# Optimization experiments

Hardware: AMD Instinct MI355X
Metric: run time of the kernel (lower is better)

The kernel has to match this reference:

```python
import jax, jax.numpy as jnp
import numpy as np

KS = (16, 16, 16)  # k per layer

def _knn_idx(pts, k):
    # pts: (P, C). Exclude self (knn_graph default loop=False).
    P = pts.shape[0]
    sq = jnp.sum(pts * pts, axis=1)
    d2 = sq[:, None] + sq[None, :] - 2.0 * (pts @ pts.T)  # (P, P)
    d2 = d2.at[jnp.arange(P), jnp.arange(P)].set(jnp.inf)
    _, idx = jax.lax.top_k(-d2, k)  # (P, k) nearest neighbors
    return idx

def _edge_conv(h, idx, W, b):
    # h: (P, C); idx: (P, k); W: (2C, Cout)
    hi = h[:, None, :]                      # (P, 1, C)
    hj = h[idx]                             # (P, k, C) gather
    msg = jnp.concatenate([jnp.broadcast_to(hi, hj.shape), hj - hi], axis=-1)
    m = msg @ W + b                         # (P, k, Cout)
    return jnp.max(m, axis=1)               # max aggregation -> (P, Cout)

def setup_inputs() -> dict:
    key = jax.random.key(0)
    ks = jax.random.split(key, 12)
    B, N, d = 2, 4096, 3
    chans = [d, 64, 128, 256]
    inp = {"x": jax.random.normal(ks[0], (B, N, d), dtype=jnp.float32)}
    for i in range(3):
        cin, cout = chans[i], chans[i + 1]
        s = 1.0 / np.sqrt(2 * cin)
        inp[f"W{i+1}"] = jax.random.uniform(ks[1 + 2 * i], (2 * cin, cout), jnp.float32, -s, s)
        inp[f"b{i+1}"] = jax.random.uniform(ks[2 + 2 * i], (cout,), jnp.float32, -s, s)
    s1 = 1.0 / np.sqrt(256.0)
    inp["fW1"] = jax.random.uniform(ks[7], (256, 128), jnp.float32, -s1, s1)
    inp["fb1"] = jax.random.uniform(ks[8], (128,), jnp.float32, -s1, s1)
    s2 = 1.0 / np.sqrt(128.0)
    inp["fW2"] = jax.random.uniform(ks[9], (128, 1), jnp.float32, -s2, s2)
    inp["fb2"] = jax.random.uniform(ks[10], (1,), jnp.float32, -s2, s2)
    return inp

def reference(x, W1, b1, W2, b2, W3, b3, fW1, fb1, fW2, fb2):
    B, N, _ = x.shape
    h = x.reshape(B * N, -1)  # KNN spans flattened batch (batch=None in source)
    for (W, b, k) in ((W1, b1, KS[0]), (W2, b2, KS[1]), (W3, b3, KS[2])):
        idx = _knn_idx(h, k)
        h = jax.nn.relu(_edge_conv(h, idx, W, b))
    out = jax.nn.relu(h @ fW1 + fb1) @ fW2 + fb2  # (P, 1)
    return out.reshape(B, N, 1)
```

## Files before the change

kernel.cpp:

```cpp
#include <hip/hip_runtime.h>
#include <hip/hip_bf16.h>

#define PTS 8192
#define NSPLIT 8

__device__ __forceinline__ void top_init(float (&bd)[16], int (&bi)[16]) {
#pragma unroll
  for (int t = 0; t < 16; ++t) { bd[t] = 3e38f; bi[t] = 0; }
}

__device__ __forceinline__ void top_insert(float (&bd)[16], int (&bi)[16], float d, int j) {
  if (d < bd[15]) {
#pragma unroll
    for (int t = 15; t >= 0; --t) {
      bool c  = d < bd[t];
      bool cp = (t > 0) ? (d < bd[t - 1]) : false;
      float nd = cp ? bd[t - 1] : d;
      int   ni = cp ? bi[t - 1] : j;
      if (c) { bd[t] = nd; bi[t] = ni; }
    }
  }
}

__global__ void sqnorm_kernel(const float* __restrict__ h, float* __restrict__ sq, int C) {
  int i = blockIdx.x * 256 + threadIdx.x;
  if (i >= PTS) return;
  const float* r = h + (size_t)i * C;
  float s = 0.f;
  if ((C & 3) == 0) {
    for (int k = 0; k < C; k += 4) {
      float4 v = *(const float4*)(r + k);
      s += v.x * v.x + v.y * v.y + v.z * v.z + v.w * v.w;
    }
  } else {
    for (int k = 0; k < C; ++k) s += r[k] * r[k];
  }
  sq[i] = s;
}

template <int C>
__global__ __launch_bounds__(128) void knn_kernel(const float* __restrict__ H,
                                                  const float* __restrict__ sq,
                                                  float* __restrict__ pd,
                                                  int* __restrict__ pi) {
  constexpr int KC = (C < 32) ? C : 32;
  constexpr int NC = C / KC;
  constexpr int TT = (PTS / NSPLIT) / 64;
  constexpr int N  = TT * NC;

  __shared__ __align__(128) float AsF[C * 64];
  __shared__ __align__(128) float S[2 * 32 * 64];

  const int tid  = threadIdx.x;
  const int b    = blockIdx.x;
  const int sy   = b & 7;
  const int sx   = b >> 3;
  const int row0 = sx * 64;
  const int cb   = sy * (PTS / NSPLIT);
  const int tx = tid & 15, ty = tid >> 4;
  const int r_ = tid & 63, g_ = tid >> 6;

  if constexpr (C >= 32) {
    const int r = tid >> 1, h = tid & 1;
#pragma unroll
    for (int j = 0; j < C / 8; ++j) {
      int q = h * (C / 8) + j;
      float4 v = *(const float4*)(H + (size_t)(row0 + r) * C + q * 4);
      float vv[4] = {v.x, v.y, v.z, v.w};
#pragma unroll
      for (int e = 0; e < 4; ++e)
        AsF[(q * 4 + e) * 64 + r] = vv[e];
    }
  } else {
    if (tid < 16 * C) {
      float4 v = *(const float4*)(H + (size_t)row0 * C + tid * 4);
      float vv[4] = {v.x, v.y, v.z, v.w};
#pragma unroll
      for (int e = 0; e < 4; ++e) {
        int gi = tid * 4 + e;
        AsF[(gi % C) * 64 + gi / C] = vv[e];
      }
    }
  }

  float sqr[8];
#pragma unroll
  for (int u = 0; u < 8; ++u) sqr[u] = sq[row0 + ty * 8 + u];

  float bd[16]; int bi[16];
  top_init(bd, bi);

  float4 st[4];
#pragma unroll
  for (int j = 0; j < 4; ++j) st[j] = make_float4(0.f, 0.f, 0.f, 0.f);

  auto stage_load = [&](int n1) {
    if constexpr (C >= 32) {
      const int c = tid & 63, kq = tid >> 6;
      const float* src = H + (size_t)(cb + (n1 / NC) * 64 + c) * C + (n1 % NC) * KC + kq * 16;
#pragma unroll
      for (int j = 0; j < 4; ++j) st[j] = *(const float4*)(src + j * 4);
    } else {
      if (tid < 16 * C) st[0] = *(const float4*)(H + (size_t)(cb + n1 * 64) * C + tid * 4);
    }
  };
  auto stage_write = [&](int n1) {
    float* B = S + (n1 & 1) * 2048;
    if constexpr (C >= 32) {
      const int c = tid & 63, kq = tid >> 6;
#pragma unroll
      for (int j = 0; j < 4; ++j) {
        float vv[4] = {st[j].x, st[j].y, st[j].z, st[j].w};
#pragma unroll
        for (int e = 0; e < 4; ++e)
          B[(kq * 16 + j * 4 + e) * 64 + c] = vv[e];
      }
    } else {
      if (tid < 16 * C) {
        float vv[4] = {st[0].x, st[0].y, st[0].z, st[0].w};
#pragma unroll
        for (int e = 0; e < 4; ++e) {
          int gi = tid * 4 + e;
          B[(gi % C) * 64 + gi / C] = vv[e];
        }
      }
    }
  };

  stage_load(0);
  stage_write(0);
  __syncthreads();

  float acc[8][4] = {};
  for (int n = 0; n < N; ++n) {
    if (n + 1 < N) stage_load(n + 1);
    const float* Bh = S + (n & 1) * 2048;
    const int kc = (n % NC) * KC;
#pragma unroll
    for (int k = 0; k < KC; ++k) {
      float4 a40 = *(const float4*)(AsF + (kc + k) * 64 + ty * 8);
      float4 a41 = *(const float4*)(AsF + (kc + k) * 64 + ty * 8 + 4);
      float4 b4  = *(const float4*)(Bh + k * 64 + tx * 4);
      float a[8]  = {a40.x, a40.y, a40.z, a40.w, a41.x, a41.y, a41.z, a41.w};
      float bb[4] = {b4.x, b4.y, b4.z, b4.w};
#pragma unroll
      for (int u = 0; u < 8; ++u)
#pragma unroll
        for (int v = 0; v < 4; ++v)
          acc[u][v] += a[u] * bb[v];
    }
    if ((n % NC) == NC - 1) {
      const int ct = (n / NC) * 64;
      const int cbase = cb + ct;
      float sqc[4];
#pragma unroll
      for (int v = 0; v < 4; ++v) sqc[v] = sq[cbase + tx * 4 + v];
      __syncthreads();
#pragma unroll
      for (int u = 0; u < 8; ++u) {
        int row = ty * 8 + u;
        int gr  = row0 + row;
        int sw  = (row & 7) << 2;
        float dv[4];
#pragma unroll
        for (int v = 0; v < 4; ++v) {
          float d2 = sqr[u] + sqc[v] - 2.f * acc[u][v];
          if (gr == cbase + tx * 4 + v) d2 = 3e38f;
          dv[v] = d2;
          acc[u][v] = 0.f;
        }
        *(float4*)(S + row * 64 + ((tx * 4) ^ sw)) = make_float4(dv[0], dv[1], dv[2], dv[3]);
      }
      __syncthreads();
      const int swr = (r_ & 7) << 2;
      unsigned mask = 0;
#pragma unroll
      for (int j = 0; j < 8; ++j) {
        float4 f = *(const float4*)(S + r_ * 64 + ((g_ * 32 + j * 4) ^ swr));
        if (f.x < bd[15]) mask |= (1u << (j * 4 + 0));
        if (f.y < bd[15]) mask |= (1u << (j * 4 + 1));
        if (f.z < bd[15]) mask |= (1u << (j * 4 + 2));
        if (f.w < bd[15]) mask |= (1u << (j * 4 + 3));
      }
      while (mask) {
        int q = __ffs(mask) - 1;
        mask &= mask - 1;
        int cc = g_ * 32 + q;
        float d = S[r_ * 64 + (cc ^ swr)];
        top_insert(bd, bi, d, cbase + cc);
      }
      __syncthreads();
    }
    if (n + 1 < N) {
      stage_write(n + 1);
      __syncthreads();
    }
  }

  __syncthreads();
  if (g_ == 1) {
    float* base = S + r_ * 32;
#pragma unroll
    for (int t = 0; t < 16; ++t) {
      int s = (t + r_) & 15;
      base[s] = bd[t];
      ((int*)base)[16 + s] = bi[t];
    }
  }
  __syncthreads();
  if (g_ == 0) {
    const float* base = S + r_ * 32;
    for (int t = 0; t < 16; ++t) {
      int s = (t + r_) & 15;
      float d = base[s];
      if (d >= bd[15]) break;
      top_insert(bd, bi, d, ((const int*)base)[16 + s]);
    }
    size_t basep = ((size_t)(row0 + r_) * NSPLIT + sy) * 16;
#pragma unroll
    for (int t = 0; t < 16; ++t) { pd[basep + t] = bd[t]; pi[basep + t] = bi[t]; }
  }
}

__global__ void knn_merge_kernel(const float* __restrict__ pd, const int* __restrict__ pi,
                                 int* __restrict__ idx) {
  int i = blockIdx.x * 256 + threadIdx.x;
  if (i >= PTS) return;
  float bd[16]; int bi[16];
  top_init(bd, bi);
  const float* d  = pd + (size_t)i * (NSPLIT * 16);
  const int*   ii = pi + (size_t)i * (NSPLIT * 16);
  for (int L = 0; L < NSPLIT; ++L) {
    for (int t = 0; t < 16; ++t) {
      float dv = d[L * 16 + t];
      if (dv >= bd[15]) break;
      top_insert(bd, bi, dv, ii[L * 16 + t]);
    }
  }
#pragma unroll
  for (int t = 0; t < 16; ++t) idx[(size_t)i * 16 + t] = bi[t];
}

__global__ __launch_bounds__(256) void gemm_fg_kernel(const float* __restrict__ A,
                                                      const float* __restrict__ Wt,
                                                      const float* __restrict__ Wb,
                                                      const float* __restrict__ bias,
                                                      float* __restrict__ F, float* __restrict__ G,
                                                      int K, int N) {
  __shared__ float As[16][68];
  __shared__ float Bs[16][68];
  const int tid  = threadIdx.x;
  const int row0 = blockIdx.x * 64, col0 = blockIdx.y * 64;
  const float* B = (blockIdx.z == 0) ? Wt : Wb;
  float* O       = (blockIdx.z == 0) ? F  : G;
  const int tx = tid & 15, ty = tid >> 4;
  float acc[4][4] = {};
  for (int k0 = 0; k0 < K; k0 += 16) {
    __syncthreads();
#pragma unroll
    for (int l = 0; l < 4; ++l) {
      int rr = (tid >> 4) + l * 16, kk = tid & 15;
      As[kk][rr] = (k0 + kk < K) ? A[(size_t)(row0 + rr) * K + k0 + kk] : 0.f;
      int cc = tid & 63, k2 = (tid >> 6) + l * 4;
      Bs[k2][cc] = (k0 + k2 < K) ? B[(size_t)(k0 + k2) * N + col0 + cc] : 0.f;
    }
    __syncthreads();
#pragma unroll
    for (int k = 0; k < 16; ++k) {
      float4 a4 = *(const float4*)&As[k][ty * 4];
      float4 b4 = *(const float4*)&Bs[k][tx * 4];
      float a[4] = {a4.x, a4.y, a4.z, a4.w};
      float b[4] = {b4.x, b4.y, b4.z, b4.w};
#pragma unroll
      for (int u = 0; u < 4; ++u)
#pragma unroll
        for (int v = 0; v < 4; ++v)
          acc[u][v] += a[u] * b[v];
    }
  }
  float bv[4] = {0.f, 0.f, 0.f, 0.f};
  if (blockIdx.z == 0) {
#pragma unroll
    for (int v = 0; v < 4; ++v) bv[v] = bias[col0 + tx * 4 + v];
  }
#pragma unroll
  for (int u = 0; u < 4; ++u)
#pragma unroll
    for (int v = 0; v < 4; ++v)
      O[(size_t)(row0 + ty * 4 + u) * N + col0 + tx * 4 + v] = acc[u][v] + bv[v];
}

__global__ void gather_max_kernel(const float* __restrict__ F, const float* __restrict__ G,
                                  const int* __restrict__ idx, float* __restrict__ Ho, int Cn) {
  int t = blockIdx.x * 256 + threadIdx.x;
  int per = Cn >> 2;
  int i = t / per;
  if (i >= PTS) return;
  int c = (t - i * per) * 4;
  const int* ji = idx + (size_t)i * 16;
  float4 m = make_float4(-3e38f, -3e38f, -3e38f, -3e38f);
#pragma unroll
  for (int s = 0; s < 16; ++s) {
    float4 v = *(const float4*)(G + (size_t)ji[s] * Cn + c);
    m.x = fmaxf(m.x, v.x); m.y = fmaxf(m.y, v.y);
    m.z = fmaxf(m.z, v.z); m.w = fmaxf(m.w, v.w);
  }
  float4 gi = *(const float4*)(G + (size_t)i * Cn + c);
  float4 f  = *(const float4*)(F + (size_t)i * Cn + c);
  float4 o;
  o.x = fmaxf(f.x - gi.x + m.x, 0.f);
  o.y = fmaxf(f.y - gi.y + m.y, 0.f);
  o.z = fmaxf(f.z - gi.z + m.z, 0.f);
  o.w = fmaxf(f.w - gi.w + m.w, 0.f);
  *(float4*)(Ho + (size_t)i * Cn + c) = o;
}

__global__ __launch_bounds__(256) void mlp_kernel(const float* __restrict__ h3,
                                                  const float* __restrict__ fW1,
                                                  const float* __restrict__ fb1,
                                                  const float* __restrict__ fW2,
                                                  const float* __restrict__ fb2,
                                                  float* __restrict__ out) {
  __shared__ float hs[16][260];
  __shared__ float ws[64][128];
  __shared__ float red[4][8];
  const int tid = threadIdx.x;
  const int p0  = blockIdx.x * 16;
#pragma unroll
  for (int l = 0; l < 16; ++l) {
    int ii = l * 256 + tid;
    hs[ii >> 8][ii & 255] = h3[(size_t)(p0 + (ii >> 8)) * 256 + (ii & 255)];
  }
  const int c = tid & 127, half = tid >> 7;
  float acc[8];
#pragma unroll
  for (int pp = 0; pp < 8; ++pp) acc[pp] = fb1[c];
  for (int k0 = 0; k0 < 256; k0 += 64) {
    __syncthreads();
#pragma unroll
    for (int l = 0; l < 32; ++l) {
      int ii = l * 256 + tid;
      ws[ii >> 7][ii & 127] = fW1[(size_t)(k0 + (ii >> 7)) * 128 + (ii & 127)];
    }
    __syncthreads();
    for (int k = 0; k < 64; k += 4) {
      float w0 = ws[k][c], w1 = ws[k + 1][c], w2 = ws[k + 2][c], w3 = ws[k + 3][c];
#pragma unroll
      for (int pp = 0; pp < 8; ++pp) {
        float4 h4 = *(const float4*)&hs[half * 8 + pp][k0 + k];
        acc[pp] += h4.x * w0 + h4.y * w1 + h4.z * w2 + h4.w * w3;
      }
    }
  }
  float w2v = fW2[c];
  float s[8];
#pragma unroll
  for (int pp = 0; pp < 8; ++pp) s[pp] = fmaxf(acc[pp], 0.f) * w2v;
#pragma unroll
  for (int off = 32; off > 0; off >>= 1) {
#pragma unroll
    for (int pp = 0; pp < 8; ++pp) s[pp] += __shfl_down(s[pp], off);
  }
  if ((tid & 63) == 0) {
#pragma unroll
    for (int pp = 0; pp < 8; ++pp) red[tid >> 6][pp] = s[pp];
  }
  __syncthreads();
  if (tid < 16) {
    int hf = tid >> 3, pp = tid & 7;
    float v = red[hf * 2][pp] + red[hf * 2 + 1][pp] + fb2[0];
    out[p0 + hf * 8 + pp] = v;
  }
}

extern "C" void kernel_launch(void* const* d_in, const int* in_sizes, int n_in,
                              void* d_out, int out_size, void* d_ws, size_t ws_size,
                              hipStream_t stream) {
  (void)in_sizes; (void)n_in; (void)out_size; (void)ws_size;
  const float* x   = (const float*)d_in[0];
  const float* W1  = (const float*)d_in[1];
  const float* b1  = (const float*)d_in[2];
  const float* W2  = (const float*)d_in[3];
  const float* b2  = (const float*)d_in[4];
  const float* W3  = (const float*)d_in[5];
  const float* b3  = (const float*)d_in[6];
  const float* fW1 = (const float*)d_in[7];
  const float* fb1 = (const float*)d_in[8];
  const float* fW2 = (const float*)d_in[9];
  const float* fb2 = (const float*)d_in[10];

  float* w = (float*)d_ws;
  size_t o = 0;
  float* sq  = w + o; o += PTS;
  float* h1  = w + o; o += (size_t)PTS * 64;
  float* h2  = w + o; o += (size_t)PTS * 128;
  float* h3  = w + o; o += (size_t)PTS * 256;
  float* F   = w + o; o += (size_t)PTS * 256;
  float* G   = w + o; o += (size_t)PTS * 256;
  float* pd  = w + o; o += (size_t)PTS * 128;
  int*   pi  = (int*)(w + o); o += (size_t)PTS * 128;
  int*   idx = (int*)(w + o); o += (size_t)PTS * 16;

  const int KNN_GRID = (PTS / 64) * NSPLIT;

  sqnorm_kernel<<<PTS / 256, 256, 0, stream>>>(x, sq, 3);
  knn_kernel<3><<<KNN_GRID, 128, 0, stream>>>(x, sq, pd, pi);
  knn_merge_kernel<<<PTS / 256, 256, 0, stream>>>(pd, pi, idx);
  gemm_fg_kernel<<<dim3(PTS / 64, 1, 2), 256, 0, stream>>>(x, W1, W1 + 3 * 64, b1, F, G, 3, 64);
  gather_max_kernel<<<(PTS * 16 + 255) / 256, 256, 0, stream>>>(F, G, idx, h1, 64);

  sqnorm_kernel<<<PTS / 256, 256, 0, stream>>>(h1, sq, 64);
  knn_kernel<64><<<KNN_GRID, 128, 0, stream>>>(h1, sq, pd, pi);
  knn_merge_kernel<<<PTS / 256, 256, 0, stream>>>(pd, pi, idx);
  gemm_fg_kernel<<<dim3(PTS / 64, 2, 2), 256, 0, stream>>>(h1, W2, W2 + 64 * 128, b2, F, G, 64, 128);
  gather_max_kernel<<<(PTS * 32 + 255) / 256, 256, 0, stream>>>(F, G, idx, h2, 128);

  sqnorm_kernel<<<PTS / 256, 256, 0, stream>>>(h2, sq, 128);
  knn_kernel<128><<<KNN_GRID, 128, 0, stream>>>(h2, sq, pd, pi);
  knn_merge_kernel<<<PTS / 256, 256, 0, stream>>>(pd, pi, idx);
  gemm_fg_kernel<<<dim3(PTS / 64, 4, 2), 256, 0, stream>>>(h2, W3, W3 + 128 * 256, b3, F, G, 128, 256);
  gather_max_kernel<<<(PTS * 64 + 255) / 256, 256, 0, stream>>>(F, G, idx, h3, 256);

  mlp_kernel<<<PTS / 16, 256, 0, stream>>>(h3, fW1, fb1, fW2, fb2, (float*)d_out);
}
```

Before: 1.022 ms.

## Halve kNN row tile to 32 rows and split candidate scan across four thread groups

```diff
diff --git a/kernel.cpp b/kernel.cpp
--- a/kernel.cpp
+++ b/kernel.cpp
@@ -43,86 +43,80 @@
                                                   const float* __restrict__ sq,
                                                   float* __restrict__ pd,
                                                   int* __restrict__ pi) {
-  constexpr int KC = (C < 32) ? C : 32;
+  constexpr int KC = (C < 16) ? C : 16;
   constexpr int NC = C / KC;
   constexpr int TT = (PTS / NSPLIT) / 64;
   constexpr int N  = TT * NC;
 
-  __shared__ __align__(128) float AsF[C * 64];
-  __shared__ __align__(128) float S[2 * 32 * 64];
+  __shared__ __align__(128) float AsF[C * 32];
+  __shared__ __align__(128) float S[2048];
 
   const int tid  = threadIdx.x;
   const int b    = blockIdx.x;
   const int sy   = b & 7;
   const int sx   = b >> 3;
-  const int row0 = sx * 64;
+  const int row0 = sx * 32;
   const int cb   = sy * (PTS / NSPLIT);
   const int tx = tid & 15, ty = tid >> 4;
-  const int r_ = tid & 63, g_ = tid >> 6;
-
-  if constexpr (C >= 32) {
-    const int r = tid >> 1, h = tid & 1;
-#pragma unroll
-    for (int j = 0; j < C / 8; ++j) {
-      int q = h * (C / 8) + j;
+  const int r_ = tid & 31, g4 = tid >> 5;
+  const int l_ = tid & 63, w_ = tid >> 6;
+
+  if constexpr (C >= 16) {
+    const int r = tid >> 2, q0 = tid & 3;
+#pragma unroll
+    for (int j = 0; j < C / 16; ++j) {
+      int q = q0 + j * 4;
       float4 v = *(const float4*)(H + (size_t)(row0 + r) * C + q * 4);
       float vv[4] = {v.x, v.y, v.z, v.w};
 #pragma unroll
       for (int e = 0; e < 4; ++e)
-        AsF[(q * 4 + e) * 64 + r] = vv[e];
+        AsF[(q * 4 + e) * 32 + r] = vv[e];
     }
   } else {
-    if (tid < 16 * C) {
-      float4 v = *(const float4*)(H + (size_t)row0 * C + tid * 4);
-      float vv[4] = {v.x, v.y, v.z, v.w};
-#pragma unroll
-      for (int e = 0; e < 4; ++e) {
-        int gi = tid * 4 + e;
-        AsF[(gi % C) * 64 + gi / C] = vv[e];
-      }
-    }
-  }
-
-  float sqr[8];
-#pragma unroll
-  for (int u = 0; u < 8; ++u) sqr[u] = sq[row0 + ty * 8 + u];
+    if (tid < 32 * C) {
+      int rr = tid & 31, kk = tid >> 5;
+      AsF[kk * 32 + rr] = H[(size_t)(row0 + rr) * C + kk];
+    }
+  }
+
+  float sqr[4];
+#pragma unroll
+  for (int u = 0; u < 4; ++u) sqr[u] = sq[row0 + ty * 4 + u];
 
   float bd[16]; int bi[16];
   top_init(bd, bi);
 
-  float4 st[4];
-#pragma unroll
-  for (int j = 0; j < 4; ++j) st[j] = make_float4(0.f, 0.f, 0.f, 0.f);
-
+  float4 st0 = make_float4(0.f, 0.f, 0.f, 0.f);
+  float4 st1 = make_float4(0.f, 0.f, 0.f, 0.f);
   auto stage_load = [&](int n1) {
-    if constexpr (C >= 32) {
+    if constexpr (C >= 16) {
       const int c = tid & 63, kq = tid >> 6;
-      const float* src = H + (size_t)(cb + (n1 / NC) * 64 + c) * C + (n1 % NC) * KC + kq * 16;
-#pragma unroll
-      for (int j = 0; j < 4; ++j) st[j] = *(const float4*)(src + j * 4);
+      const float* src = H + (size_t)(cb + (n1 / NC) * 64 + c) * C + (n1 % NC) * KC + kq * 8;
+      st0 = *(const float4*)(src);
+      st1 = *(const float4*)(src + 4);
     } else {
-      if (tid < 16 * C) st[0] = *(const float4*)(H + (size_t)(cb + n1 * 64) * C + tid * 4);
+      if (tid < 64) {
+        const float* src = H + (size_t)(cb + n1 * 64 + tid) * C;
+        st0.x = src[0]; st0.y = src[1]; st0.z = src[2];
+      }
     }
   };
   auto stage_write = [&](int n1) {
-    float* B = S + (n1 & 1) * 2048;
-    if constexpr (C >= 32) {
+    float* B = S + (n1 & 1) * 1024;
+    if constexpr (C >= 16) {
       const int c = tid & 63, kq = tid >> 6;
-#pragma unroll
-      for (int j = 0; j < 4; ++j) {
-        float vv[4] = {st[j].x, st[j].y, st[j].z, st[j].w};
-#pragma unroll
-        for (int e = 0; e < 4; ++e)
-          B[(kq * 16 + j * 4 + e) * 64 + c] = vv[e];
+      float v0[4] = {st0.x, st0.y, st0.z, st0.w};
+      float v1[4] = {st1.x, st1.y, st1.z, st1.w};
+#pragma unroll
+      for (int e = 0; e < 4; ++e) {
+        B[(kq * 8 + e) * 64 + c]     = v0[e];
+        B[(kq * 8 + 4 + e) * 64 + c] = v1[e];
       }
     } else {
-      if (tid < 16 * C) {
-        float vv[4] = {st[0].x, st[0].y, st[0].z, st[0].w};
-#pragma unroll
-        for (int e = 0; e < 4; ++e) {
-          int gi = tid * 4 + e;
-          B[(gi % C) * 64 + gi / C] = vv[e];
-        }
+      if (tid < 64) {
+        B[0 * 64 + tid] = st0.x;
+        B[1 * 64 + tid] = st0.y;
+        B[2 * 64 + tid] = st0.z;
       }
     }
   };
@@ -131,20 +125,19 @@
   stage_write(0);
   __syncthreads();
 
-  float acc[8][4] = {};
+  float acc[4][4] = {};
   for (int n = 0; n < N; ++n) {
     if (n + 1 < N) stage_load(n + 1);
-    const float* Bh = S + (n & 1) * 2048;
+    const float* Bh = S + (n & 1) * 1024;
     const int kc = (n % NC) * KC;
 #pragma unroll
     for (int k = 0; k < KC; ++k) {
-      float4 a40 = *(const float4*)(AsF + (kc + k) * 64 + ty * 8);
-      float4 a41 = *(const float4*)(AsF + (kc + k) * 64 + ty * 8 + 4);
-      float4 b4  = *(const float4*)(Bh + k * 64 + tx * 4);
-      float a[8]  = {a40.x, a40.y, a40.z, a40.w, a41.x, a41.y, a41.z, a41.w};
+      float4 a4 = *(const float4*)(AsF + (kc + k) * 32 + ty * 4);
+      float4 b4 = *(const float4*)(Bh + k * 64 + tx * 4);
+      float a[4]  = {a4.x, a4.y, a4.z, a4.w};
       float bb[4] = {b4.x, b4.y, b4.z, b4.w};
 #pragma unroll
-      for (int u = 0; u < 8; ++u)
+      for (int u = 0; u < 4; ++u)
 #pragma unroll
         for (int v = 0; v < 4; ++v)
           acc[u][v] += a[u] * bb[v];
@@ -157,8 +150,8 @@
       for (int v = 0; v < 4; ++v) sqc[v] = sq[cbase + tx * 4 + v];
       __syncthreads();
 #pragma unroll
-      for (int u = 0; u < 8; ++u) {
-        int row = ty * 8 + u;
+      for (int u = 0; u < 4; ++u) {
+        int row = ty * 4 + u;
         int gr  = row0 + row;
         int sw  = (row & 7) << 2;
         float dv[4];
@@ -175,8 +168,8 @@
       const int swr = (r_ & 7) << 2;
       unsigned mask = 0;
 #pragma unroll
-      for (int j = 0; j < 8; ++j) {
-        float4 f = *(const float4*)(S + r_ * 64 + ((g_ * 32 + j * 4) ^ swr));
+      for (int j = 0; j < 4; ++j) {
+        float4 f = *(const float4*)(S + r_ * 64 + ((g4 * 16 + j * 4) ^ swr));
         if (f.x < bd[15]) mask |= (1u << (j * 4 + 0));
         if (f.y < bd[15]) mask |= (1u << (j * 4 + 1));
         if (f.z < bd[15]) mask |= (1u << (j * 4 + 2));
@@ -185,7 +178,7 @@
       while (mask) {
         int q = __ffs(mask) - 1;
         mask &= mask - 1;
-        int cc = g_ * 32 + q;
+        int cc = g4 * 16 + q;
         float d = S[r_ * 64 + (cc ^ swr)];
         top_insert(bd, bi, d, cbase + cc);
       }
@@ -197,8 +190,15 @@
     }
   }
 
+  for (int t = 0; t < 16; ++t) {
+    float d = __shfl(bd[t], (l_ & 31) + 32);
+    int   i = __shfl(bi[t], (l_ & 31) + 32);
+    unsigned long long m = __ballot((l_ < 32) && (d < bd[15]));
+    if (!m) break;
+    if (l_ < 32) top_insert(bd, bi, d, i);
+  }
   __syncthreads();
-  if (g_ == 1) {
+  if (w_ == 1 && l_ < 32) {
     float* base = S + r_ * 32;
 #pragma unroll
     for (int t = 0; t < 16; ++t) {
@@ -208,7 +208,7 @@
     }
   }
   __syncthreads();
-  if (g_ == 0) {
+  if (w_ == 0 && l_ < 32) {
     const float* base = S + r_ * 32;
     for (int t = 0; t < 16; ++t) {
       int s = (t + r_) & 15;
@@ -401,7 +401,7 @@
   int*   pi  = (int*)(w + o); o += (size_t)PTS * 128;
   int*   idx = (int*)(w + o); o += (size_t)PTS * 16;
 
-  const int KNN_GRID = (PTS / 64) * NSPLIT;
+  const int KNN_GRID = (PTS / 32) * NSPLIT;
 
   sqnorm_kernel<<<PTS / 256, 256, 0, stream>>>(x, sq, 3);
   knn_kernel<3><<<KNN_GRID, 128, 0, stream>>>(x, sq, pd, pi);
```

Result: faster. 959.2 us (-6.2%).
